# Kernel optimization log

Hardware: AMD Instinct MI355X
Metric: run time of the kernel (lower is better)

## Reference

```python
import jax, jax.numpy as jnp
import numpy as np

N, B, M, K, C = 120000, 8, 60000, 16, 32
EX = 512  # 128 * expansion_factor 4
EPS = 1e-5


def _bn(h, g, b):
    # BatchNorm1d (training-mode batch stats, biased var), stats over points
    m = h.mean(axis=0)
    v = h.var(axis=0)
    return (h - m) * jax.lax.rsqrt(v + EPS) * g + b


def setup_inputs() -> dict:
    key = jax.random.key(0)
    ks = jax.random.split(key, 20)

    def w(i, shape, fan):
        return jax.random.normal(ks[i], shape, jnp.float32) / np.sqrt(fan)

    inp = {}
    inp["x"] = jax.random.normal(ks[0], (N, C), jnp.float32)
    inp["pos"] = jax.random.normal(ks[1], (N, 3), jnp.float32) * 5.0
    inp["batch"] = jnp.sort(jax.random.randint(ks[2], (N,), 0, B))
    inp["reflectance"] = jax.random.uniform(ks[3], (N,), jnp.float32)
    inp["sf"] = jax.random.uniform(ks[4], (B,), jnp.float32, minval=0.5, maxval=1.5)
    inp["idx"] = jnp.sort(jax.random.randint(ks[5], (M,), 0, N))
    inp["edge_src"] = jax.random.randint(ks[6], (M * K,), 0, N)
    inp["edge_dst"] = jnp.repeat(jnp.arange(M), K)
    # local_nn MLP channels [C+4, 64, 64, 128]; first layer has no BN
    inp["mlp_W1"] = w(7, (C + 4, 64), C + 4); inp["mlp_b1"] = jnp.zeros((64,))
    inp["mlp_W2"] = w(8, (64, 64), 64); inp["mlp_b2"] = jnp.zeros((64,))
    inp["mlp_g2"] = jnp.ones((64,)); inp["mlp_be2"] = jnp.zeros((64,))
    inp["mlp_W3"] = w(9, (64, 128), 64); inp["mlp_b3"] = jnp.zeros((128,))
    inp["mlp_g3"] = jnp.ones((128,)); inp["mlp_be3"] = jnp.zeros((128,))
    # ReflectanceYesNo (1 -> 32 -> 32 -> 1)
    inp["ryn_W1"] = w(10, (1, 32), 1); inp["ryn_b1"] = jnp.zeros((32,))
    inp["ryn_W2"] = w(11, (32, 32), 32); inp["ryn_b2"] = jnp.zeros((32,))
    inp["ryn_W3"] = w(12, (32, 1), 32); inp["ryn_b3"] = jnp.zeros((1,))
    # InvertedResidualBlock 128 -> 512 -> 128 (all 1x1 convs)
    inp["exp_W"] = w(13, (128, EX), 128); inp["exp_b"] = jnp.zeros((EX,))
    inp["exp_g"] = jnp.ones((EX,)); inp["exp_be"] = jnp.zeros((EX,))
    inp["dw_w"] = jax.random.normal(ks[14], (2, EX), jnp.float32)  # depthwise k=1 -> per-channel scale
    inp["dw_b"] = jnp.zeros((2, EX)); inp["dw_g"] = jnp.ones((2, EX)); inp["dw_be"] = jnp.zeros((2, EX))
    inp["pw_W"] = w(15, (2, EX, EX), EX); inp["pw_b"] = jnp.zeros((2, EX))
    inp["pw_g"] = jnp.ones((2, EX)); inp["pw_be"] = jnp.zeros((2, EX))
    inp["c_g"] = jnp.ones((2, EX)); inp["c_be"] = jnp.zeros((2, EX))
    inp["proj_W"] = w(16, (EX, 128), EX); inp["proj_b"] = jnp.zeros((128,))
    inp["proj_g"] = jnp.ones((128,)); inp["proj_be"] = jnp.zeros((128,))
    return inp


def reference(x, pos, batch, reflectance, sf, idx, edge_src, edge_dst,
              mlp_W1, mlp_b1, mlp_W2, mlp_b2, mlp_g2, mlp_be2, mlp_W3, mlp_b3, mlp_g3, mlp_be3,
              ryn_W1, ryn_b1, ryn_W2, ryn_b2, ryn_W3, ryn_b3,
              exp_W, exp_b, exp_g, exp_be, dw_w, dw_b, dw_g, dw_be,
              pw_W, pw_b, pw_g, pw_be, c_g, c_be, proj_W, proj_b, proj_g, proj_be):
    Bn = sf.shape[0]
    Mn = idx.shape[0]
    pos4 = jnp.concatenate([pos[:, :3], reflectance[:, None]], axis=-1)  # [N,4]

    # --- ReflectanceYesNo gating (gumbel_softmax over a size-1 axis == ones, straight-through) ---
    h = jax.nn.relu(reflectance[:, None] @ ryn_W1 + ryn_b1)
    h = jax.nn.relu(h @ ryn_W2 + ryn_b2)
    pooled = jax.ops.segment_sum(h, batch, num_segments=Bn)
    counts = jax.ops.segment_sum(jnp.ones((h.shape[0],), h.dtype), batch, num_segments=Bn)
    logits = (pooled / counts[:, None]) @ ryn_W3 + ryn_b3  # [B,1]
    y_soft = jax.nn.softmax(logits, axis=-1)               # size-1 softmax -> all ones
    y = jax.lax.stop_gradient(jnp.ones_like(y_soft) - y_soft) + y_soft
    gate = jnp.where(jnp.sum(reflectance) != 0.0, y[:, 0][batch], 1.0)
    refl4 = pos4[:, 3] * gate

    # --- scale coords, PointNetConv: gather -> local_nn MLP -> max aggregate ---
    scale = sf[batch][:, None]
    pos_s = jnp.concatenate([pos4[:, :3] / scale, refl4[:, None]], axis=-1)  # [N,4]
    rel = pos_s[edge_src] - pos_s[idx][edge_dst]                              # [E,4]
    msg = jnp.concatenate([x[edge_src], rel], axis=-1)                        # [E,C+4]
    h1 = jax.nn.relu(msg @ mlp_W1 + mlp_b1)
    h2 = _bn(jax.nn.relu(h1 @ mlp_W2 + mlp_b2), mlp_g2, mlp_be2)
    h3 = _bn(jax.nn.relu(h2 @ mlp_W3 + mlp_b3), mlp_g3, mlp_be3)
    agg = jax.ops.segment_max(h3, edge_dst, num_segments=Mn)                  # [M,128]
    agg = jnp.where(jnp.isneginf(agg), 0.0, agg)  # PyG fills isolated nodes with 0

    # --- InvertedResidualBlock (1x1 convs == per-point linears, BN over points) ---
    res = agg
    e = jax.nn.relu(_bn(agg @ exp_W + exp_b, exp_g, exp_be))

    def ds(hh, i):  # DepthwiseSeparableConv1d, k=1
        d = jax.nn.relu(_bn(hh * dw_w[i] + dw_b[i], dw_g[i], dw_be[i]))
        return jax.nn.relu(_bn(d @ pw_W[i] + pw_b[i], pw_g[i], pw_be[i]))

    cmid = jax.nn.relu(_bn(ds(e, 0), c_g[0], c_be[0]))
    cmid = _bn(ds(cmid, 1), c_g[1], c_be[1])
    o = _bn(cmid @ proj_W + proj_b, proj_g, proj_be)
    out = jax.nn.relu(o + res)  # shortcut is identity (in == out channels)

    return (out, pos[idx, :3], batch[idx], reflectance[idx], sf)
```

## Files before the change

### kernel.cpp

```cpp
#include <hip/hip_runtime.h>
#include <hip/hip_bf16.h>
#include <cstdint>

#define DEV_INLINE __device__ __forceinline__

typedef unsigned short u16;
typedef unsigned int   u32;
typedef short bf16x8 __attribute__((ext_vector_type(8)));
typedef float f32x4  __attribute__((ext_vector_type(4)));

#define AS_GLOBAL(p) ((const __attribute__((address_space(1))) void*)(p))
#define AS_LDS(p)    ((__attribute__((address_space(3))) void*)(p))

constexpr int NP = 120000, NB = 8, NM = 60000, KNN = 16;
constexpr int NE = NM * KNN;
constexpr float EPS = 1e-5f;

constexpr size_t O_POS   = (size_t)NM * 128;
constexpr size_t O_BATCH = O_POS + (size_t)NM * 3;
constexpr size_t O_REFL  = O_BATCH + NM;
constexpr size_t O_SF    = O_REFL + NM;

__device__ float  g_pos_s[(size_t)NP * 4];
__device__ u16    g_xbf[(size_t)NP * 32];
__device__ u16    g_pre2[(size_t)NE * 64];
__device__ u32    g_mm[(size_t)NM * 128];
__device__ float  g_agg[(size_t)NM * 128];
__device__ u16    g_aggbf[(size_t)NM * 128];
__device__ u16    g_bufA[(size_t)NM * 512];
__device__ u16    g_bufB[(size_t)NM * 512];
__device__ float  g_obuf[(size_t)NM * 128];
__device__ float  g_sum[512], g_sqs[512], g_cfa[512], g_cfb[512];
__device__ float  g_b3adj[128], g_pbadj[128];
__device__ u16 g_w1t[64 * 64];
__device__ u16 g_w2t[64 * 64];
__device__ u16 g_w3t[128 * 64];
__device__ u16 g_expwt[512 * 128];
__device__ u16 g_pw0t[512 * 512];
__device__ u16 g_pw1t[512 * 512];
__device__ u16 g_projwt[128 * 512];

template<int ID> DEV_INLINE const u16* ubufsel() {
  if constexpr (ID == 1) return g_aggbf;
  else if constexpr (ID == 2) return g_bufA;
  else return g_bufB;
}
template<int ID> DEV_INLINE u16* obufsel() {
  if constexpr (ID == 2) return g_bufA;
  else return g_bufB;
}
template<int ID> DEV_INLINE const u16* wsel() {
  if constexpr (ID == 3) return g_expwt;
  else if constexpr (ID == 4) return g_pw0t;
  else if constexpr (ID == 5) return g_pw1t;
  else return g_projwt;
}

DEV_INLINE float bf2f(u16 u) { u32 x = (u32)u << 16; float f; __builtin_memcpy(&f, &x, 4); return f; }
DEV_INLINE u16 f2bf(float f) {
  u32 x; __builtin_memcpy(&x, &f, 4);
  return (u16)((x + 0x7FFFu + ((x >> 16) & 1u)) >> 16);
}
DEV_INLINE u32 pack2(float a, float b) { return (u32)f2bf(a) | ((u32)f2bf(b) << 16); }

__global__ void prep_pos_x(const float* __restrict__ pos, const int* __restrict__ batch,
                           const float* __restrict__ refl, const float* __restrict__ sf,
                           const float* __restrict__ x) {
  int i = blockIdx.x * blockDim.x + threadIdx.x;
  if (i >= NP) return;
  float s = sf[batch[i]];
  float4 v;
  v.x = pos[(size_t)i*3+0] / s;
  v.y = pos[(size_t)i*3+1] / s;
  v.z = pos[(size_t)i*3+2] / s;
  v.w = refl[i];
  *reinterpret_cast<float4*>(g_pos_s + (size_t)i*4) = v;
  const float4* xr = reinterpret_cast<const float4*>(x + (size_t)i*32);
#pragma unroll
  for (int q = 0; q < 4; q++) {
    float4 a = xr[q*2], b = xr[q*2+1];
    uint4 u = make_uint4(pack2(a.x,a.y), pack2(a.z,a.w), pack2(b.x,b.y), pack2(b.z,b.w));
    *reinterpret_cast<uint4*>(g_xbf + (size_t)i*32 + q*8) = u;
  }
}

__global__ void tail_out(const float* __restrict__ pos, const int* __restrict__ batch,
                         const float* __restrict__ refl, const float* __restrict__ sf,
                         const int* __restrict__ idx, float* __restrict__ out) {
  int i = blockIdx.x * blockDim.x + threadIdx.x;
  if (i < NM) {
    int p = idx[i];
    out[O_POS + (size_t)i*3+0] = pos[(size_t)p*3+0];
    out[O_POS + (size_t)i*3+1] = pos[(size_t)p*3+1];
    out[O_POS + (size_t)i*3+2] = pos[(size_t)p*3+2];
    out[O_BATCH + i] = (float)batch[p];
    out[O_REFL  + i] = refl[p];
  }
  if (i < NB) out[O_SF + i] = sf[i];
}

__global__ void zero_stats() {
  int t = threadIdx.x;
  g_sum[t] = 0.f; g_sqs[t] = 0.f;
}

__global__ void prep_weights(const float* __restrict__ W1, const float* __restrict__ W2,
                             const float* __restrict__ W3, const float* __restrict__ expW,
                             const float* __restrict__ pwW, const float* __restrict__ projW) {
  int i = blockIdx.x * 256 + threadIdx.x;
  const int s0 = 4096, s1 = 4096, s2 = 8192, s3 = 65536, s4 = 262144, s5 = 262144, s6 = 65536;
  if (i < s0) { int n = i >> 6, k = i & 63; g_w1t[i] = (k < 36) ? f2bf(W1[k*64 + n]) : (u16)0; return; }
  i -= s0;
  if (i < s1) { int n = i >> 6, k = i & 63; g_w2t[i] = f2bf(W2[k*64 + n]); return; }
  i -= s1;
  if (i < s2) { int n = i >> 6, k = i & 63; g_w3t[i] = f2bf(W3[k*128 + n]); return; }
  i -= s2;
  if (i < s3) { int n = i >> 7, k = i & 127; g_expwt[i] = f2bf(expW[k*512 + n]); return; }
  i -= s3;
  if (i < s4) { int n = i >> 9, k = i & 511; g_pw0t[i] = f2bf(pwW[k*512 + n]); return; }
  i -= s4;
  if (i < s5) { int n = i >> 9, k = i & 511; g_pw1t[i] = f2bf(pwW[262144 + k*512 + n]); return; }
  i -= s5;
  if (i < s6) { int n = i >> 9, k = i & 511; g_projwt[i] = f2bf(projW[k*128 + n]); return; }
}

__global__ void param_bn(const float* __restrict__ g, const float* __restrict__ be,
                         float n, int C) {
  int c = threadIdx.x;
  if (c < C) {
    float mean = g_sum[c] / n;
    float var  = fmaxf(g_sqs[c] / n - mean * mean, 0.f);
    float a = g[c] * rsqrtf(var + EPS);
    g_cfa[c] = a;
    g_cfb[c] = be[c] - a * mean;
  }
  __syncthreads();
  g_sum[c] = 0.f; g_sqs[c] = 0.f;
}

__global__ void param_dw(const float* __restrict__ w, const float* __restrict__ g,
                         const float* __restrict__ be, float n, int C) {
  int c = threadIdx.x;
  if (c < C) {
    float mean = g_sum[c] / n;
    float var  = fmaxf(g_sqs[c] / n - mean * mean, 0.f);
    float r = rsqrtf(w[c]*w[c]*var + EPS);
    float a = w[c] * r * g[c];
    g_cfa[c] = a;
    g_cfb[c] = be[c] - a * mean;
  }
  __syncthreads();
  g_sum[c] = 0.f; g_sqs[c] = 0.f;
}

template<int SID>
__global__ void scale_fold(const float* __restrict__ bias_in, int N, int K) {
  u16* Wt = (SID == 0) ? g_w3t : g_projwt;
  float* badj = (SID == 0) ? g_b3adj : g_pbadj;
  int w = (blockIdx.x * blockDim.x + threadIdx.x) >> 6;
  int lane = threadIdx.x & 63;
  if (w >= N) return;
  float acc = 0.f;
  for (int k = lane; k < K; k += 64) {
    float wv = bf2f(Wt[(size_t)w*K + k]);
    acc = fmaf(g_cfb[k], wv, acc);
    Wt[(size_t)w*K + k] = f2bf(g_cfa[k] * wv);
  }
#pragma unroll
  for (int o = 32; o; o >>= 1) acc += __shfl_xor(acc, o, 64);
  if (lane == 0) badj[w] = bias_in[w] + acc;
}

constexpr int K1_BLOCKS = 960;
__launch_bounds__(256)
__global__ void k1_edge(const int* __restrict__ esrc, const int* __restrict__ idx,
                        const float* __restrict__ b1v, const float* __restrict__ b2v) {
  __shared__ u16 sH[4][16][72];
  __shared__ float ssum[64], ssqs[64];
  const int tid = threadIdx.x;
  if (tid < 64) { ssum[tid] = 0.f; ssqs[tid] = 0.f; }
  __syncthreads();
  const int w = tid >> 6, lane = tid & 63, l15 = lane & 15, l4 = lane >> 4;
  u16 (*sh)[72] = sH[w];
  bf16x8 w1f[2][4], w2f[2][4];
#pragma unroll
  for (int ks = 0; ks < 2; ks++)
#pragma unroll
    for (int fc = 0; fc < 4; fc++) {
      w1f[ks][fc] = *reinterpret_cast<const bf16x8*>(g_w1t + (size_t)(fc*16+l15)*64 + ks*32 + l4*8);
      w2f[ks][fc] = *reinterpret_cast<const bf16x8*>(g_w2t + (size_t)(fc*16+l15)*64 + ks*32 + l4*8);
    }
  float b1r[4], b2r[4];
#pragma unroll
  for (int fc = 0; fc < 4; fc++) { b1r[fc] = b1v[fc*16+l15]; b2r[fc] = b2v[fc*16+l15]; }
  float s8[4] = {}, q8[4] = {};
  const int t0 = blockIdx.x * 4 + w;
  const int TSTRIDE = K1_BLOCKS * 4;
  int   s_cur = esrc[t0*16 + l15];
  uint4 x_cur = *reinterpret_cast<const uint4*>(g_xbf + (size_t)s_cur*32 + l4*8);
  float4 ps_cur = make_float4(0.f,0.f,0.f,0.f);
  if (l4 == 0) ps_cur = *reinterpret_cast<const float4*>(g_pos_s + (size_t)s_cur*4);
  float4 pc_cur = *reinterpret_cast<const float4*>(g_pos_s + (size_t)idx[t0]*4);

  for (int t = t0; t < NM; t += TSTRIDE) {
    const int tn = t + TSTRIDE;
    int s_nx = 0; uint4 x_nx = make_uint4(0,0,0,0);
    float4 ps_nx = ps_cur, pc_nx = pc_cur;
    if (tn < NM) {
      s_nx = esrc[tn*16 + l15];
      x_nx = *reinterpret_cast<const uint4*>(g_xbf + (size_t)s_nx*32 + l4*8);
      if (l4 == 0) ps_nx = *reinterpret_cast<const float4*>(g_pos_s + (size_t)s_nx*4);
      pc_nx = *reinterpret_cast<const float4*>(g_pos_s + (size_t)idx[tn]*4);
    }
    bf16x8 a0 = __builtin_bit_cast(bf16x8, x_cur);
    uint4 r4 = make_uint4(0,0,0,0);
    if (l4 == 0) {
      r4.x = pack2(ps_cur.x - pc_cur.x, ps_cur.y - pc_cur.y);
      r4.y = pack2(ps_cur.z - pc_cur.z, ps_cur.w - pc_cur.w);
    }
    bf16x8 a1 = __builtin_bit_cast(bf16x8, r4);
    f32x4 acc1[4] = {};
#pragma unroll
    for (int fc = 0; fc < 4; fc++) {
      acc1[fc] = __builtin_amdgcn_mfma_f32_16x16x32_bf16(a0, w1f[0][fc], acc1[fc], 0, 0, 0);
      acc1[fc] = __builtin_amdgcn_mfma_f32_16x16x32_bf16(a1, w1f[1][fc], acc1[fc], 0, 0, 0);
    }
#pragma unroll
    for (int fc = 0; fc < 4; fc++)
#pragma unroll
      for (int r = 0; r < 4; r++)
        sh[l4*4 + r][fc*16 + l15] = f2bf(fmaxf(acc1[fc][r] + b1r[fc], 0.f));
    bf16x8 h0  = *reinterpret_cast<const bf16x8*>(&sh[l15][l4*8]);
    bf16x8 h1v = *reinterpret_cast<const bf16x8*>(&sh[l15][32 + l4*8]);
    f32x4 acc2[4] = {};
#pragma unroll
    for (int fc = 0; fc < 4; fc++) {
      acc2[fc] = __builtin_amdgcn_mfma_f32_16x16x32_bf16(h0,  w2f[0][fc], acc2[fc], 0, 0, 0);
      acc2[fc] = __builtin_amdgcn_mfma_f32_16x16x32_bf16(h1v, w2f[1][fc], acc2[fc], 0, 0, 0);
    }
#pragma unroll
    for (int fc = 0; fc < 4; fc++)
#pragma unroll
      for (int r = 0; r < 4; r++) {
        float v = fmaxf(acc2[fc][r] + b2r[fc], 0.f);
        s8[fc] += v; q8[fc] += v*v;
        sh[l4*4 + r][fc*16 + l15] = f2bf(v);
      }
    uint4 p0 = *reinterpret_cast<const uint4*>(&sh[l15][l4*8]);
    uint4 p1 = *reinterpret_cast<const uint4*>(&sh[l15][32 + l4*8]);
    *reinterpret_cast<uint4*>(g_pre2 + (size_t)t*1024 + lane*8)       = p0;
    *reinterpret_cast<uint4*>(g_pre2 + (size_t)t*1024 + 512 + lane*8) = p1;
    s_cur = s_nx; x_cur = x_nx; ps_cur = ps_nx; pc_cur = pc_nx;
  }
#pragma unroll
  for (int fc = 0; fc < 4; fc++) {
    float sv = s8[fc], qv = q8[fc];
    sv += __shfl_xor(sv, 16, 64); sv += __shfl_xor(sv, 32, 64);
    qv += __shfl_xor(qv, 16, 64); qv += __shfl_xor(qv, 32, 64);
    if (l4 == 0) { atomicAdd(&ssum[fc*16 + l15], sv); atomicAdd(&ssqs[fc*16 + l15], qv); }
  }
  __syncthreads();
  if (tid < 64) { atomicAdd(&g_sum[tid], ssum[tid]); atomicAdd(&g_sqs[tid], ssqs[tid]); }
}

constexpr int K2_BLOCKS = 960;
__launch_bounds__(256)
__global__ void k2_edge() {
  __shared__ float ssum[128], ssqs[128];
  const int tid = threadIdx.x;
  if (tid < 128) { ssum[tid] = 0.f; ssqs[tid] = 0.f; }
  __syncthreads();
  const int lane = tid & 63, l15 = lane & 15, l4 = lane >> 4;
  const int wglobal = blockIdx.x * 4 + (tid >> 6);
  const int WSTRIDE = K2_BLOCKS * 4;
  bf16x8 w3f[2][8];
#pragma unroll
  for (int ks = 0; ks < 2; ks++)
#pragma unroll
    for (int fc = 0; fc < 8; fc++)
      w3f[ks][fc] = *reinterpret_cast<const bf16x8*>(g_w3t + (size_t)(fc*16 + l15)*64 + ks*32 + l4*8);
  float bv[8];
#pragma unroll
  for (int fc = 0; fc < 8; fc++) bv[fc] = g_b3adj[fc*16 + l15];
  float s[8] = {}, q[8] = {};
  int t = wglobal;
  uint4 an0 = make_uint4(0,0,0,0), an1 = an0;
  if (t < NM) {
    const uint4* p = reinterpret_cast<const uint4*>(g_pre2 + (size_t)t*1024 + lane*8);
    an0 = p[0]; an1 = p[64];
  }
  for (; t < NM; t += WSTRIDE) {
    uint4 a0 = an0, a1 = an1;
    int tn = t + WSTRIDE;
    if (tn < NM) {
      const uint4* p = reinterpret_cast<const uint4*>(g_pre2 + (size_t)tn*1024 + lane*8);
      an0 = p[0]; an1 = p[64];
    }
    bf16x8 af0 = __builtin_bit_cast(bf16x8, a0);
    bf16x8 af1 = __builtin_bit_cast(bf16x8, a1);
    f32x4 acc[8] = {};
#pragma unroll
    for (int fc = 0; fc < 8; fc++) {
      acc[fc] = __builtin_amdgcn_mfma_f32_16x16x32_bf16(af0, w3f[0][fc], acc[fc], 0, 0, 0);
      acc[fc] = __builtin_amdgcn_mfma_f32_16x16x32_bf16(af1, w3f[1][fc], acc[fc], 0, 0, 0);
    }
    u32 rbase = (u32)t * 128u;
#pragma unroll
    for (int fc = 0; fc < 8; fc++) {
      float v0 = fmaxf(acc[fc][0] + bv[fc], 0.f);
      float v1 = fmaxf(acc[fc][1] + bv[fc], 0.f);
      float v2 = fmaxf(acc[fc][2] + bv[fc], 0.f);
      float v3 = fmaxf(acc[fc][3] + bv[fc], 0.f);
      s[fc] += (v0 + v1) + (v2 + v3);
      q[fc] += (v0*v0 + v1*v1) + (v2*v2 + v3*v3);
      float mx = fmaxf(fmaxf(v0, v1), fmaxf(v2, v3));
      float mn = fminf(fminf(v0, v1), fminf(v2, v3));
      mx = fmaxf(mx, __shfl_xor(mx, 16, 64)); mx = fmaxf(mx, __shfl_xor(mx, 32, 64));
      mn = fminf(mn, __shfl_xor(mn, 16, 64)); mn = fminf(mn, __shfl_xor(mn, 32, 64));
      if (l4 == (fc & 3))
        g_mm[rbase + fc*16 + l15] = (u32)f2bf(mx) | ((u32)f2bf(mn) << 16);
    }
  }
#pragma unroll
  for (int fc = 0; fc < 8; fc++) {
    float sv = s[fc], qv = q[fc];
    sv += __shfl_xor(sv, 16, 64); sv += __shfl_xor(sv, 32, 64);
    qv += __shfl_xor(qv, 16, 64); qv += __shfl_xor(qv, 32, 64);
    if (l4 == 0) { atomicAdd(&ssum[fc*16 + l15], sv); atomicAdd(&ssqs[fc*16 + l15], qv); }
  }
  __syncthreads();
  if (tid < 128) { atomicAdd(&g_sum[tid], ssum[tid]); atomicAdd(&g_sqs[tid], ssqs[tid]); }
}

__global__ void k3_agg() {
  int i4 = (blockIdx.x * 256 + threadIdx.x) * 4;
  if (i4 >= NM * 128) return;
  int c = i4 & 127;
  uint4 mm = *reinterpret_cast<const uint4*>(g_mm + i4);
  float4 a = *reinterpret_cast<const float4*>(g_cfa + c);
  float4 b = *reinterpret_cast<const float4*>(g_cfb + c);
  u32 u[4] = {mm.x, mm.y, mm.z, mm.w};
  float av[4] = {a.x, a.y, a.z, a.w};
  float bb[4] = {b.x, b.y, b.z, b.w};
  float4 r;
  float* rr = &r.x;
#pragma unroll
  for (int j = 0; j < 4; j++) {
    float mx = bf2f((u16)(u[j] & 0xFFFFu));
    float mn = bf2f((u16)(u[j] >> 16));
    rr[j] = av[j] > 0.f ? fmaf(av[j], mx, bb[j]) : fmaf(av[j], mn, bb[j]);
  }
  *reinterpret_cast<float4*>(g_agg + i4) = r;
  uint2 pk; pk.x = pack2(r.x, r.y); pk.y = pack2(r.z, r.w);
  *reinterpret_cast<uint2*>(g_aggbf + i4) = pk;
}

template<int AID, int WID, int OID, int NPAN, bool OUT_BF16, bool BIAS_DEV>
__launch_bounds__(256, 4)
__global__ void gemm_mfma(const float* __restrict__ bias, int Mrows, int Kdim) {
  const int Ncols = NPAN * 128;
  const u16* __restrict__ A  = ubufsel<AID>();
  const u16* __restrict__ Bt = wsel<WID>();
  __shared__ u16 sLDS[16384];
  __shared__ float ssum[128], ssqs[128];
  u16* sA = sLDS;
  u16* sB = sLDS + 8192;
  const int tid = threadIdx.x;
  const int bid = blockIdx.x;
  const int m0 = (bid / NPAN) * 128, n0 = (bid % NPAN) * 128;
  if (tid < 128) { ssum[tid] = 0.f; ssqs[tid] = 0.f; }
  const int wave = tid >> 6, lane = tid & 63, l15 = lane & 15, l4 = lane >> 4;
  const int wr = wave >> 1, wc = wave & 1;
  const int ckk = (lane & 3) * 8;
  f32x4 acc[4][4] = {};
  const int nt = Kdim >> 5;

  auto STAGE = [&](int buf, int t) {
    const int k0 = t * 32;
#pragma unroll
    for (int i = 0; i < 2; i++) {
      const int c = wave * 2 + i;
      int ar = m0 + c * 16 + (lane >> 2);
      if (ar >= Mrows) ar = Mrows - 1;
      const int br = n0 + c * 16 + (lane >> 2);
      __builtin_amdgcn_global_load_lds(AS_GLOBAL(A  + (size_t)ar * Kdim + k0 + ckk),
                                       AS_LDS(sA + buf*4096 + c*512), 16, 0, 0);
      __builtin_amdgcn_global_load_lds(AS_GLOBAL(Bt + (size_t)br * Kdim + k0 + ckk),
                                       AS_LDS(sB + buf*4096 + c*512), 16, 0, 0);
    }
  };

  STAGE(0, 0);
  __syncthreads();
  int cur = 0;
  for (int t = 0; t < nt; ++t) {
    if (t + 1 < nt) STAGE(cur ^ 1, t + 1);
    bf16x8 af[4], bf4[4];
#pragma unroll
    for (int fr = 0; fr < 4; fr++) {
      int r = wr*64 + fr*16 + l15;
      af[fr] = *reinterpret_cast<const bf16x8*>(sA + cur*4096 + r*32 + l4*8);
    }
#pragma unroll
    for (int fc = 0; fc < 4; fc++) {
      int r = wc*64 + fc*16 + l15;
      bf4[fc] = *reinterpret_cast<const bf16x8*>(sB + cur*4096 + r*32 + l4*8);
    }
#pragma unroll
    for (int fr = 0; fr < 4; fr++)
#pragma unroll
      for (int fc = 0; fc < 4; fc++)
        acc[fr][fc] = __builtin_amdgcn_mfma_f32_16x16x32_bf16(af[fr], bf4[fc], acc[fr][fc], 0, 0, 0);
    if (t + 1 < nt) { __syncthreads(); cur ^= 1; }
  }

  __syncthreads();
  const int orow = m0 + wr*64 + l4*4;
#pragma unroll
  for (int fc = 0; fc < 4; fc++) {
    int col = n0 + wc*64 + fc*16 + l15;
    float bvv = BIAS_DEV ? g_pbadj[col] : bias[col];
    float s = 0.f, q = 0.f;
#pragma unroll
    for (int fr = 0; fr < 4; fr++)
#pragma unroll
      for (int r = 0; r < 4; r++) {
        int row = orow + fr*16 + r;
        if (row < Mrows) {
          float v = acc[fr][fc][r] + bvv;
          s += v; q += v*v;
          if (OUT_BF16) sLDS[(size_t)(wr*64 + fr*16 + l4*4 + r)*128 + wc*64 + fc*16 + l15] = f2bf(v);
          else          g_obuf[(size_t)row*Ncols + col] = v;
        }
      }
    atomicAdd(&ssum[wc*64 + fc*16 + l15], s);
    atomicAdd(&ssqs[wc*64 + fc*16 + l15], q);
  }
  __syncthreads();
  if (OUT_BF16) {
    const int r2 = tid >> 1, hh = tid & 1;
    if (m0 + r2 < Mrows) {
      const uint4* src = reinterpret_cast<const uint4*>(sLDS + r2*128 + hh*64);
      uint4* dst = reinterpret_cast<uint4*>(obufsel<OID>() + (size_t)(m0 + r2)*Ncols + n0 + hh*64);
#pragma unroll
      for (int j = 0; j < 8; j++) dst[j] = src[j];
    }
  }
  if (tid < 128) { atomicAdd(&g_sum[n0 + tid], ssum[tid]); atomicAdd(&g_sqs[n0 + tid], ssqs[tid]); }
}

template<int INID, int OUTID>
__launch_bounds__(256)
__global__ void ew_stats(int rows) {
  const u16* __restrict__ X = ubufsel<INID>();
  u16* __restrict__ Y = obufsel<OUTID>();
  __shared__ float ssum[512], ssqs[512];
  const int tid = threadIdx.x;
  ssum[tid] = 0.f; ssum[tid+256] = 0.f; ssqs[tid] = 0.f; ssqs[tid+256] = 0.f;
  __syncthreads();
  const int c0 = (tid & 63) * 8;
  const int rl = tid >> 6;
  float a[8], b[8];
#pragma unroll
  for (int j = 0; j < 8; j++) { a[j] = g_cfa[c0+j]; b[j] = g_cfb[c0+j]; }
  float s[8] = {}, q[8] = {};
  for (int r = blockIdx.x*4 + rl; r < rows; r += gridDim.x*4) {
    uint4 v = *reinterpret_cast<const uint4*>(X + (size_t)r*512 + c0);
    u32 u[4] = {v.x, v.y, v.z, v.w}, o[4];
#pragma unroll
    for (int t = 0; t < 4; t++) {
      float lo = bf2f((u16)(u[t] & 0xFFFFu));
      float hi = bf2f((u16)(u[t] >> 16));
      lo = fmaxf(fmaf(a[2*t],   lo, b[2*t]),   0.f);
      hi = fmaxf(fmaf(a[2*t+1], hi, b[2*t+1]), 0.f);
      s[2*t] += lo; q[2*t] += lo*lo; s[2*t+1] += hi; q[2*t+1] += hi*hi;
      o[t] = (u32)f2bf(lo) | ((u32)f2bf(hi) << 16);
    }
    *reinterpret_cast<uint4*>(Y + (size_t)r*512 + c0) = make_uint4(o[0], o[1], o[2], o[3]);
  }
#pragma unroll
  for (int j = 0; j < 8; j++) { atomicAdd(&ssum[c0+j], s[j]); atomicAdd(&ssqs[c0+j], q[j]); }
  __syncthreads();
  atomicAdd(&g_sum[tid],     ssum[tid]);     atomicAdd(&g_sqs[tid],     ssqs[tid]);
  atomicAdd(&g_sum[tid+256], ssum[tid+256]); atomicAdd(&g_sqs[tid+256], ssqs[tid+256]);
}

template<int INID, int OUTID>
__launch_bounds__(256)
__global__ void ew_apply(int rows) {
  const u16* __restrict__ X = ubufsel<INID>();
  u16* __restrict__ Y = obufsel<OUTID>();
  const int tid = threadIdx.x;
  const int c0 = (tid & 63) * 8;
  const int rl = tid >> 6;
  float a[8], b[8];
#pragma unroll
  for (int j = 0; j < 8; j++) { a[j] = g_cfa[c0+j]; b[j] = g_cfb[c0+j]; }
  for (int r = blockIdx.x*4 + rl; r < rows; r += gridDim.x*4) {
    uint4 v = *reinterpret_cast<const uint4*>(X + (size_t)r*512 + c0);
    u32 u[4] = {v.x, v.y, v.z, v.w}, o[4];
#pragma unroll
    for (int t = 0; t < 4; t++) {
      float lo = bf2f((u16)(u[t] & 0xFFFFu));
      float hi = bf2f((u16)(u[t] >> 16));
      lo = fmaxf(fmaf(a[2*t],   lo, b[2*t]),   0.f);
      hi = fmaxf(fmaf(a[2*t+1], hi, b[2*t+1]), 0.f);
      o[t] = (u32)f2bf(lo) | ((u32)f2bf(hi) << 16);
    }
    *reinterpret_cast<uint4*>(Y + (size_t)r*512 + c0) = make_uint4(o[0], o[1], o[2], o[3]);
  }
}

__global__ void final_out(float* __restrict__ out) {
  int i4 = (blockIdx.x * 256 + threadIdx.x) * 4;
  if (i4 >= NM * 128) return;
  int c = i4 & 127;
  float4 o  = *reinterpret_cast<const float4*>(g_obuf + i4);
  float4 ag = *reinterpret_cast<const float4*>(g_agg + i4);
  float4 a  = *reinterpret_cast<const float4*>(g_cfa + c);
  float4 b  = *reinterpret_cast<const float4*>(g_cfb + c);
  float4 r;
  r.x = fmaxf(fmaf(a.x, o.x, b.x) + ag.x, 0.f);
  r.y = fmaxf(fmaf(a.y, o.y, b.y) + ag.y, 0.f);
  r.z = fmaxf(fmaf(a.z, o.z, b.z) + ag.z, 0.f);
  r.w = fmaxf(fmaf(a.w, o.w, b.w) + ag.w, 0.f);
  *reinterpret_cast<float4*>(out + i4) = r;
}

extern "C" void kernel_launch(void* const* d_in, const int* in_sizes, int n_in,
                              void* d_out, int out_size, void* d_ws, size_t ws_size,
                              hipStream_t stream) {
  const float* x     = (const float*)d_in[0];
  const float* pos   = (const float*)d_in[1];
  const int*   batch = (const int*)  d_in[2];
  const float* refl  = (const float*)d_in[3];
  const float* sf    = (const float*)d_in[4];
  const int*   idx   = (const int*)  d_in[5];
  const int*   esrc  = (const int*)  d_in[6];
  const float* W1  = (const float*)d_in[8];
  const float* b1  = (const float*)d_in[9];
  const float* W2  = (const float*)d_in[10];
  const float* b2  = (const float*)d_in[11];
  const float* g2  = (const float*)d_in[12];
  const float* be2 = (const float*)d_in[13];
  const float* W3  = (const float*)d_in[14];
  const float* b3  = (const float*)d_in[15];
  const float* g3  = (const float*)d_in[16];
  const float* be3 = (const float*)d_in[17];
  const float* expW  = (const float*)d_in[24];
  const float* expb  = (const float*)d_in[25];
  const float* expg  = (const float*)d_in[26];
  const float* expbe = (const float*)d_in[27];
  const float* dww  = (const float*)d_in[28];
  const float* dwg  = (const float*)d_in[30];
  const float* dwbe = (const float*)d_in[31];
  const float* pwW  = (const float*)d_in[32];
  const float* pwb  = (const float*)d_in[33];
  const float* pwg  = (const float*)d_in[34];
  const float* pwbe = (const float*)d_in[35];
  const float* cg   = (const float*)d_in[36];
  const float* cbe  = (const float*)d_in[37];
  const float* projW  = (const float*)d_in[38];
  const float* projb  = (const float*)d_in[39];
  const float* projg  = (const float*)d_in[40];
  const float* projbe = (const float*)d_in[41];
  float* out = (float*)d_out;

  const float fNE = (float)NE, fNM = (float)NM;

  prep_weights<<<2624, 256, 0, stream>>>(W1, W2, W3, expW, pwW, projW);
  prep_pos_x<<<(NP + 255)/256, 256, 0, stream>>>(pos, batch, refl, sf, x);
  tail_out<<<(NM + 255)/256, 256, 0, stream>>>(pos, batch, refl, sf, idx, out);
  zero_stats<<<1, 512, 0, stream>>>();

  k1_edge<<<K1_BLOCKS, 256, 0, stream>>>(esrc, idx, b1, b2);
  param_bn<<<1, 512, 0, stream>>>(g2, be2, fNE, 64);
  scale_fold<0><<<32, 256, 0, stream>>>(b3, 128, 64);
  k2_edge<<<K2_BLOCKS, 256, 0, stream>>>();
  param_bn<<<1, 512, 0, stream>>>(g3, be3, fNE, 128);
  k3_agg<<<NM*128/1024, 256, 0, stream>>>();

  gemm_mfma<1, 3, 2, 4, true, false><<<469*4, 256, 0, stream>>>(expb, NM, 128);
  param_bn<<<1, 512, 0, stream>>>(expg, expbe, fNM, 512);
  ew_stats<2, 2><<<1024, 256, 0, stream>>>(NM);
  param_dw<<<1, 512, 0, stream>>>(dww, dwg, dwbe, fNM, 512);
  ew_apply<2, 3><<<1024, 256, 0, stream>>>(NM);
  gemm_mfma<3, 4, 2, 4, true, false><<<469*4, 256, 0, stream>>>(pwb, NM, 512);
  param_bn<<<1, 512, 0, stream>>>(pwg, pwbe, fNM, 512);
  ew_stats<2, 2><<<1024, 256, 0, stream>>>(NM);
  param_bn<<<1, 512, 0, stream>>>(cg, cbe, fNM, 512);
  ew_stats<2, 2><<<1024, 256, 0, stream>>>(NM);
  param_dw<<<1, 512, 0, stream>>>(dww + 512, dwg + 512, dwbe + 512, fNM, 512);
  ew_apply<2, 3><<<1024, 256, 0, stream>>>(NM);
  gemm_mfma<3, 5, 2, 4, true, false><<<469*4, 256, 0, stream>>>(pwb + 512, NM, 512);
  param_bn<<<1, 512, 0, stream>>>(pwg + 512, pwbe + 512, fNM, 512);
  ew_stats<2, 2><<<1024, 256, 0, stream>>>(NM);
  param_bn<<<1, 512, 0, stream>>>(cg + 512, cbe + 512, fNM, 512);
  scale_fold<1><<<32, 256, 0, stream>>>(projb, 128, 512);
  gemm_mfma<2, 6, 0, 1, false, true><<<469, 256, 0, stream>>>(projb, NM, 512);
  param_bn<<<1, 512, 0, stream>>>(projg, projbe, fNM, 128);
  final_out<<<NM*128/1024, 256, 0, stream>>>(out);
}
```

Before: 708.4 us.

## Chain BN-ReLU stages in registers to skip intermediate activation writes

Stores the per-channel BN coefficients in three separate slots so that consecutive BN+ReLU stages can be recomputed inside one elementwise kernel. Stats-only passes now read bufA and skip writing, and the apply pass runs two or three chained affine+ReLU steps at once, so intermediate 60000x512 bf16 tensors are no longer written. The edge kernels and elementwise grids are also doubled in size. In exchange, the chained steps are recomputed from bf16 inputs without intermediate rounding, which shifts numerics slightly.

```diff
diff --git a/kernel.cpp b/kernel.cpp
--- a/kernel.cpp
+++ b/kernel.cpp
@@ -30,7 +30,10 @@
 __device__ u16    g_bufA[(size_t)NM * 512];
 __device__ u16    g_bufB[(size_t)NM * 512];
 __device__ float  g_obuf[(size_t)NM * 128];
-__device__ float  g_sum[512], g_sqs[512], g_cfa[512], g_cfb[512];
+__device__ float  g_sum[512], g_sqs[512];
+__device__ float  g_cfa[512],  g_cfb[512];
+__device__ float  g_cfa2[512], g_cfb2[512];
+__device__ float  g_cfa3[512], g_cfb3[512];
 __device__ float  g_b3adj[128], g_pbadj[128];
 __device__ u16 g_w1t[64 * 64];
 __device__ u16 g_w2t[64 * 64];
@@ -54,6 +57,12 @@
   else if constexpr (ID == 4) return g_pw0t;
   else if constexpr (ID == 5) return g_pw1t;
   else return g_projwt;
+}
+template<int BK> DEV_INLINE float* cfaP() {
+  if constexpr (BK == 1) return g_cfa; else if constexpr (BK == 2) return g_cfa2; else return g_cfa3;
+}
+template<int BK> DEV_INLINE float* cfbP() {
+  if constexpr (BK == 1) return g_cfb; else if constexpr (BK == 2) return g_cfb2; else return g_cfb3;
 }
 
 DEV_INLINE float bf2f(u16 u) { u32 x = (u32)u << 16; float f; __builtin_memcpy(&f, &x, 4); return f; }
@@ -124,6 +133,7 @@
   if (i < s6) { int n = i >> 9, k = i & 511; g_projwt[i] = f2bf(projW[k*128 + n]); return; }
 }
 
+template<int BK>
 __global__ void param_bn(const float* __restrict__ g, const float* __restrict__ be,
                          float n, int C) {
   int c = threadIdx.x;
@@ -131,13 +141,14 @@
     float mean = g_sum[c] / n;
     float var  = fmaxf(g_sqs[c] / n - mean * mean, 0.f);
     float a = g[c] * rsqrtf(var + EPS);
-    g_cfa[c] = a;
-    g_cfb[c] = be[c] - a * mean;
+    cfaP<BK>()[c] = a;
+    cfbP<BK>()[c] = be[c] - a * mean;
   }
   __syncthreads();
   g_sum[c] = 0.f; g_sqs[c] = 0.f;
 }
 
+template<int BK>
 __global__ void param_dw(const float* __restrict__ w, const float* __restrict__ g,
                          const float* __restrict__ be, float n, int C) {
   int c = threadIdx.x;
@@ -146,8 +157,8 @@
     float var  = fmaxf(g_sqs[c] / n - mean * mean, 0.f);
     float r = rsqrtf(w[c]*w[c]*var + EPS);
     float a = w[c] * r * g[c];
-    g_cfa[c] = a;
-    g_cfb[c] = be[c] - a * mean;
+    cfaP<BK>()[c] = a;
+    cfbP<BK>()[c] = be[c] - a * mean;
   }
   __syncthreads();
   g_sum[c] = 0.f; g_sqs[c] = 0.f;
@@ -171,7 +182,7 @@
   if (lane == 0) badj[w] = bias_in[w] + acc;
 }
 
-constexpr int K1_BLOCKS = 960;
+constexpr int K1_BLOCKS = 1920;
 __launch_bounds__(256)
 __global__ void k1_edge(const int* __restrict__ esrc, const int* __restrict__ idx,
                         const float* __restrict__ b1v, const float* __restrict__ b2v) {
@@ -263,7 +274,7 @@
   if (tid < 64) { atomicAdd(&g_sum[tid], ssum[tid]); atomicAdd(&g_sqs[tid], ssqs[tid]); }
 }
 
-constexpr int K2_BLOCKS = 960;
+constexpr int K2_BLOCKS = 1920;
 __launch_bounds__(256)
 __global__ void k2_edge() {
   __shared__ float ssum[128], ssqs[128];
@@ -449,20 +460,26 @@
   if (tid < 128) { atomicAdd(&g_sum[n0 + tid], ssum[tid]); atomicAdd(&g_sqs[n0 + tid], ssqs[tid]); }
 }
 
-template<int INID, int OUTID>
+template<int INID, int OUTID, int NCH, bool WRITE, bool STATS>
 __launch_bounds__(256)
-__global__ void ew_stats(int rows) {
+__global__ void ew_chain(int rows) {
   const u16* __restrict__ X = ubufsel<INID>();
   u16* __restrict__ Y = obufsel<OUTID>();
   __shared__ float ssum[512], ssqs[512];
   const int tid = threadIdx.x;
-  ssum[tid] = 0.f; ssum[tid+256] = 0.f; ssqs[tid] = 0.f; ssqs[tid+256] = 0.f;
-  __syncthreads();
+  if (STATS) {
+    ssum[tid] = 0.f; ssum[tid+256] = 0.f; ssqs[tid] = 0.f; ssqs[tid+256] = 0.f;
+    __syncthreads();
+  }
   const int c0 = (tid & 63) * 8;
   const int rl = tid >> 6;
-  float a[8], b[8];
-#pragma unroll
-  for (int j = 0; j < 8; j++) { a[j] = g_cfa[c0+j]; b[j] = g_cfb[c0+j]; }
+  float a1[8], b1[8], a2[8], b2[8], a3[8], b3[8];
+#pragma unroll
+  for (int j = 0; j < 8; j++) {
+    a1[j] = g_cfa[c0+j]; b1[j] = g_cfb[c0+j];
+    if constexpr (NCH >= 2) { a2[j] = g_cfa2[c0+j]; b2[j] = g_cfb2[c0+j]; }
+    if constexpr (NCH >= 3) { a3[j] = g_cfa3[c0+j]; b3[j] = g_cfb3[c0+j]; }
+  }
   float s[8] = {}, q[8] = {};
   for (int r = blockIdx.x*4 + rl; r < rows; r += gridDim.x*4) {
     uint4 v = *reinterpret_cast<const uint4*>(X + (size_t)r*512 + c0);
@@ -471,43 +488,27 @@
     for (int t = 0; t < 4; t++) {
       float lo = bf2f((u16)(u[t] & 0xFFFFu));
       float hi = bf2f((u16)(u[t] >> 16));
-      lo = fmaxf(fmaf(a[2*t],   lo, b[2*t]),   0.f);
-      hi = fmaxf(fmaf(a[2*t+1], hi, b[2*t+1]), 0.f);
-      s[2*t] += lo; q[2*t] += lo*lo; s[2*t+1] += hi; q[2*t+1] += hi*hi;
-      o[t] = (u32)f2bf(lo) | ((u32)f2bf(hi) << 16);
-    }
-    *reinterpret_cast<uint4*>(Y + (size_t)r*512 + c0) = make_uint4(o[0], o[1], o[2], o[3]);
-  }
-#pragma unroll
-  for (int j = 0; j < 8; j++) { atomicAdd(&ssum[c0+j], s[j]); atomicAdd(&ssqs[c0+j], q[j]); }
-  __syncthreads();
-  atomicAdd(&g_sum[tid],     ssum[tid]);     atomicAdd(&g_sqs[tid],     ssqs[tid]);
-  atomicAdd(&g_sum[tid+256], ssum[tid+256]); atomicAdd(&g_sqs[tid+256], ssqs[tid+256]);
-}
-
-template<int INID, int OUTID>
-__launch_bounds__(256)
-__global__ void ew_apply(int rows) {
-  const u16* __restrict__ X = ubufsel<INID>();
-  u16* __restrict__ Y = obufsel<OUTID>();
-  const int tid = threadIdx.x;
-  const int c0 = (tid & 63) * 8;
-  const int rl = tid >> 6;
-  float a[8], b[8];
-#pragma unroll
-  for (int j = 0; j < 8; j++) { a[j] = g_cfa[c0+j]; b[j] = g_cfb[c0+j]; }
-  for (int r = blockIdx.x*4 + rl; r < rows; r += gridDim.x*4) {
-    uint4 v = *reinterpret_cast<const uint4*>(X + (size_t)r*512 + c0);
-    u32 u[4] = {v.x, v.y, v.z, v.w}, o[4];
-#pragma unroll
-    for (int t = 0; t < 4; t++) {
-      float lo = bf2f((u16)(u[t] & 0xFFFFu));
-      float hi = bf2f((u16)(u[t] >> 16));
-      lo = fmaxf(fmaf(a[2*t],   lo, b[2*t]),   0.f);
-      hi = fmaxf(fmaf(a[2*t+1], hi, b[2*t+1]), 0.f);
-      o[t] = (u32)f2bf(lo) | ((u32)f2bf(hi) << 16);
-    }
-    *reinterpret_cast<uint4*>(Y + (size_t)r*512 + c0) = make_uint4(o[0], o[1], o[2], o[3]);
+      lo = fmaxf(fmaf(a1[2*t],   lo, b1[2*t]),   0.f);
+      hi = fmaxf(fmaf(a1[2*t+1], hi, b1[2*t+1]), 0.f);
+      if constexpr (NCH >= 2) {
+        lo = fmaxf(fmaf(a2[2*t],   lo, b2[2*t]),   0.f);
+        hi = fmaxf(fmaf(a2[2*t+1], hi, b2[2*t+1]), 0.f);
+      }
+      if constexpr (NCH >= 3) {
+        lo = fmaxf(fmaf(a3[2*t],   lo, b3[2*t]),   0.f);
+        hi = fmaxf(fmaf(a3[2*t+1], hi, b3[2*t+1]), 0.f);
+      }
+      if (STATS) { s[2*t] += lo; q[2*t] += lo*lo; s[2*t+1] += hi; q[2*t+1] += hi*hi; }
+      if (WRITE) o[t] = (u32)f2bf(lo) | ((u32)f2bf(hi) << 16);
+    }
+    if (WRITE) *reinterpret_cast<uint4*>(Y + (size_t)r*512 + c0) = make_uint4(o[0], o[1], o[2], o[3]);
+  }
+  if (STATS) {
+#pragma unroll
+    for (int j = 0; j < 8; j++) { atomicAdd(&ssum[c0+j], s[j]); atomicAdd(&ssqs[c0+j], q[j]); }
+    __syncthreads();
+    atomicAdd(&g_sum[tid],     ssum[tid]);     atomicAdd(&g_sqs[tid],     ssqs[tid]);
+    atomicAdd(&g_sum[tid+256], ssum[tid+256]); atomicAdd(&g_sqs[tid+256], ssqs[tid+256]);
   }
 }
 
@@ -574,30 +575,30 @@
   zero_stats<<<1, 512, 0, stream>>>();
 
   k1_edge<<<K1_BLOCKS, 256, 0, stream>>>(esrc, idx, b1, b2);
-  param_bn<<<1, 512, 0, stream>>>(g2, be2, fNE, 64);
+  param_bn<1><<<1, 512, 0, stream>>>(g2, be2, fNE, 64);
   scale_fold<0><<<32, 256, 0, stream>>>(b3, 128, 64);
   k2_edge<<<K2_BLOCKS, 256, 0, stream>>>();
-  param_bn<<<1, 512, 0, stream>>>(g3, be3, fNE, 128);
+  param_bn<1><<<1, 512, 0, stream>>>(g3, be3, fNE, 128);
   k3_agg<<<NM*128/1024, 256, 0, stream>>>();
 
   gemm_mfma<1, 3, 2, 4, true, false><<<469*4, 256, 0, stream>>>(expb, NM, 128);
-  param_bn<<<1, 512, 0, stream>>>(expg, expbe, fNM, 512);
-  ew_stats<2, 2><<<1024, 256, 0, stream>>>(NM);
-  param_dw<<<1, 512, 0, stream>>>(dww, dwg, dwbe, fNM, 512);
-  ew_apply<2, 3><<<1024, 256, 0, stream>>>(NM);
+  param_bn<1><<<1, 512, 0, stream>>>(expg, expbe, fNM, 512);
+  ew_chain<2, 3, 1, false, true><<<2048, 256, 0, stream>>>(NM);
+  param_dw<2><<<1, 512, 0, stream>>>(dww, dwg, dwbe, fNM, 512);
+  ew_chain<2, 3, 2, true, false><<<2048, 256, 0, stream>>>(NM);
   gemm_mfma<3, 4, 2, 4, true, false><<<469*4, 256, 0, stream>>>(pwb, NM, 512);
-  param_bn<<<1, 512, 0, stream>>>(pwg, pwbe, fNM, 512);
-  ew_stats<2, 2><<<1024, 256, 0, stream>>>(NM);
-  param_bn<<<1, 512, 0, stream>>>(cg, cbe, fNM, 512);
-  ew_stats<2, 2><<<1024, 256, 0, stream>>>(NM);
-  param_dw<<<1, 512, 0, stream>>>(dww + 512, dwg + 512, dwbe + 512, fNM, 512);
-  ew_apply<2, 3><<<1024, 256, 0, stream>>>(NM);
+  param_bn<1><<<1, 512, 0, stream>>>(pwg, pwbe, fNM, 512);
+  ew_chain<2, 3, 1, false, true><<<2048, 256, 0, stream>>>(NM);
+  param_bn<2><<<1, 512, 0, stream>>>(cg, cbe, fNM, 512);
+  ew_chain<2, 3, 2, false, true><<<2048, 256, 0, stream>>>(NM);
+  param_dw<3><<<1, 512, 0, stream>>>(dww + 512, dwg + 512, dwbe + 512, fNM, 512);
+  ew_chain<2, 3, 3, true, false><<<2048, 256, 0, stream>>>(NM);
   gemm_mfma<3, 5, 2, 4, true, false><<<469*4, 256, 0, stream>>>(pwb + 512, NM, 512);
-  param_bn<<<1, 512, 0, stream>>>(pwg + 512, pwbe + 512, fNM, 512);
-  ew_stats<2, 2><<<1024, 256, 0, stream>>>(NM);
-  param_bn<<<1, 512, 0, stream>>>(cg + 512, cbe + 512, fNM, 512);
+  param_bn<1><<<1, 512, 0, stream>>>(pwg + 512, pwbe + 512, fNM, 512);
+  ew_chain<2, 2, 1, true, true><<<2048, 256, 0, stream>>>(NM);
+  param_bn<1><<<1, 512, 0, stream>>>(cg + 512, cbe + 512, fNM, 512);
   scale_fold<1><<<32, 256, 0, stream>>>(projb, 128, 512);
   gemm_mfma<2, 6, 0, 1, false, true><<<469, 256, 0, stream>>>(projb, NM, 512);
-  param_bn<<<1, 512, 0, stream>>>(projg, projbe, fNM, 128);
+  param_bn<1><<<1, 512, 0, stream>>>(projg, projbe, fNM, 128);
   final_out<<<NM*128/1024, 256, 0, stream>>>(out);
 }
```

Measured after the change: 800.6 us. +13.0%, slower.
